# Kernel optimization log

Measured on AMD Instinct MI355X. Metric: run time of the kernel, lower is better.

Reference implementation:

```python
import jax, jax.numpy as jnp
import numpy as np

N = 16384; E = 262144; B = 8
IN = 768; HID = 256; H1 = 4; OUT = 128; H2 = 2

def setup_inputs() -> dict:
    key = jax.random.key(0)
    ks = jax.random.split(key, 16)
    s = 0.02
    def p(k, shape):
        return jax.random.normal(k, shape, jnp.float32) * s
    return {
        "x": jax.random.normal(ks[0], (N, IN), jnp.float32),
        "edge_index": jax.random.randint(ks[1], (2, E), 0, N),
        "batch": jnp.sort(jax.random.randint(ks[2], (N,), 0, B)),
        "W1": p(ks[3], (H1 * HID, IN)),
        "a_src1": p(ks[4], (H1, HID)),
        "a_dst1": p(ks[5], (H1, HID)),
        "b1": jnp.zeros((H1 * HID,), jnp.float32),
        "W2": p(ks[6], (H2 * OUT, H1 * HID)),
        "a_src2": p(ks[7], (H2, OUT)),
        "a_dst2": p(ks[8], (H2, OUT)),
        "b2": jnp.zeros((OUT,), jnp.float32),
        "proj_W": p(ks[9], (768, OUT)),
        "proj_b": jnp.zeros((768,), jnp.float32),
        "ln_g": jnp.ones((768,), jnp.float32),
        "ln_b": jnp.zeros((768,), jnp.float32),
        "rh_W1": p(ks[10], (32, OUT + 2)),
        "rh_b1": jnp.zeros((32,), jnp.float32),
        "rh_W2": p(ks[11], (1, 32)),
        "rh_b2": jnp.zeros((1,), jnp.float32),
        "num_graphs": B,
    }

def _gat(x, src, dst, W, a_s, a_d, bias, heads, ch, concat, n):
    # PyG GATConv (shared src/dst lin): h = x W^T -> [n, heads, ch]
    h = (x @ W.T).reshape(n, heads, ch)
    al_s = (h * a_s).sum(-1)  # [n, heads]
    al_d = (h * a_d).sum(-1)
    e = jax.nn.leaky_relu(al_s[src] + al_d[dst], 0.2)  # [E', heads]
    # segment softmax over incoming edges of each destination node
    m = jax.lax.stop_gradient(jax.ops.segment_max(e, dst, num_segments=n))
    ex = jnp.exp(e - m[dst])
    den = jax.ops.segment_sum(ex, dst, num_segments=n)
    w = ex / (den[dst] + 1e-16)
    out = jax.ops.segment_sum(w[:, :, None] * h[src], dst, num_segments=n)
    if concat:
        return out.reshape(n, heads * ch) + bias
    return out.mean(1) + bias

def reference(x, edge_index, batch, W1, a_src1, a_dst1, b1, W2, a_src2, a_dst2, b2,
              proj_W, proj_b, ln_g, ln_b, rh_W1, rh_b1, rh_W2, rh_b2, num_graphs):
    n = x.shape[0]
    src0, dst0 = edge_index[0], edge_index[1]
    loop = jnp.arange(n)  # GATConv adds self-loops by default
    src = jnp.concatenate([src0, loop])
    dst = jnp.concatenate([dst0, loop])
    h1 = jax.nn.elu(_gat(x, src, dst, W1, a_src1, a_dst1, b1, H1, HID, True, n))
    h2 = jax.nn.elu(_gat(h1, src, dst, W2, a_src2, a_dst2, b2, H2, OUT, False, n))
    # global mean pool per graph
    n_g = jax.ops.segment_sum(jnp.ones((n,), x.dtype), batch, num_segments=num_graphs)
    pooled = jax.ops.segment_sum(h2, batch, num_segments=num_graphs) / jnp.maximum(n_g, 1.0)[:, None]
    pe = pooled @ proj_W.T + proj_b
    mu = pe.mean(-1, keepdims=True)
    var = pe.var(-1, keepdims=True)
    struct_embed = (pe - mu) / jnp.sqrt(var + 1e-5) * ln_g + ln_b
    # topology stats from ORIGINAL edges (no self-loops), per original code
    e_g = jax.ops.segment_sum(jnp.ones((src0.shape[0],), x.dtype), batch[src0], num_segments=num_graphs)
    stats = jnp.stack([e_g / (n_g + 1e-6), jnp.log(n_g + 1.0)], axis=-1)  # [B, 2]
    ri = jnp.concatenate([pooled, stats], axis=-1)
    hid = jax.nn.relu(ri @ rh_W1.T + rh_b1)
    prop_risk = jax.nn.sigmoid(hid @ rh_W2.T + rh_b2)[:, 0]
    return struct_embed, h2, prop_risk
```

## Files before the change

kernel.cpp:

```cpp
#include <hip/hip_runtime.h>
#include <math.h>

#define NN    16384
#define EE    262144
#define ET    (EE + NN)
#define NB    8
#define IN_F  768
#define HID1  256
#define H1    4
#define D1    (H1*HID1)
#define OUT2  128
#define H2    2
#define D2    (H2*OUT2)

typedef __attribute__((ext_vector_type(8))) _Float16 f16x8;
typedef __attribute__((ext_vector_type(4))) float f32x4;

__device__ __forceinline__ float hf2f(unsigned short u) {
    union { unsigned short u; _Float16 h; } c; c.u = u; return (float)c.h;
}
__device__ __forceinline__ unsigned short f2hf(float f) {
    union { unsigned short u; _Float16 h; } c; c.h = (_Float16)f; return c.u;
}


__global__ void hist_kernel(const int* __restrict__ ei, const int* __restrict__ batch,
                            int* __restrict__ deg, int* __restrict__ n_g, int* __restrict__ e_cnt) {
    __shared__ int le[NB], ln[NB];
    int tid = threadIdx.x;
    if (tid < NB) { le[tid] = 0; ln[tid] = 0; }
    __syncthreads();
    int t = blockIdx.x * blockDim.x + tid;
    if (t < EE) {
        int s = ei[t];
        int d = ei[EE + t];
        atomicAdd(&deg[d], 1);
        atomicAdd(&le[batch[s]], 1);
    }
    if (t < NN) {
        atomicAdd(&ln[batch[t]], 1);
    }
    __syncthreads();
    if (tid < NB) {
        if (le[tid]) atomicAdd(&e_cnt[tid], le[tid]);
        if (ln[tid]) atomicAdd(&n_g[tid], ln[tid]);
    }
}

__global__ __launch_bounds__(1024) void scan_kernel(const int* __restrict__ deg, int* __restrict__ row_ptr) {
    __shared__ int sums[1024];
    int t = threadIdx.x;
    int base = t * 16;
    int local[16];
    int acc = 0;
#pragma unroll
    for (int i = 0; i < 16; i++) { local[i] = acc; acc += deg[base + i] + 1; }
    sums[t] = acc;
    __syncthreads();
    for (int off = 1; off < 1024; off <<= 1) {
        int v = (t >= off) ? sums[t - off] : 0;
        __syncthreads();
        sums[t] += v;
        __syncthreads();
    }
    int prev = (t == 0) ? 0 : sums[t - 1];
#pragma unroll
    for (int i = 0; i < 16; i++) row_ptr[base + i] = prev + local[i];
    if (t == 1023) row_ptr[NN] = sums[1023];
}

__global__ void scatter_kernel(const int* __restrict__ ei, const int* __restrict__ row_ptr,
                               int* __restrict__ cursor, int* __restrict__ colidx) {
    int t = blockIdx.x * blockDim.x + threadIdx.x;
    if (t >= ET) return;
    int s, d;
    if (t < EE) { s = ei[t]; d = ei[EE + t]; }
    else        { s = d = t - EE; }
    int pos = row_ptr[d] + atomicAdd(&cursor[d], 1);
    colidx[pos] = s;
}


__global__ void tohalf3_kernel(const float* __restrict__ x,  unsigned short* __restrict__ xo,
                               const float* __restrict__ w1, unsigned short* __restrict__ w1o,
                               const float* __restrict__ w2, unsigned short* __restrict__ w2o) {
    const int n1 = NN * IN_F / 4;
    const int n2 = D1 * IN_F / 4;
    const int n3 = D2 * D1 / 4;
    int i = blockIdx.x * blockDim.x + threadIdx.x;
    const float* src; unsigned short* dst; int j;
    if (i < n1)           { src = x;  dst = xo;  j = i; }
    else if (i < n1 + n2) { src = w1; dst = w1o; j = i - n1; }
    else if (i < n1 + n2 + n3) { src = w2; dst = w2o; j = i - n1 - n2; }
    else return;
    float4 v = ((const float4*)src)[j];
    ushort4 h;
    h.x = f2hf(v.x); h.y = f2hf(v.y); h.z = f2hf(v.z); h.w = f2hf(v.w);
    ((ushort4*)dst)[j] = h;
}


__device__ __forceinline__ void ld_lds16(const unsigned short* g, unsigned short* l) {
    __builtin_amdgcn_global_load_lds((__attribute__((address_space(1))) void*)g,
                                     (__attribute__((address_space(3))) void*)l, 16, 0, 0);
}

#define BM 128
#define BN 128
#define BK 32

__global__ __launch_bounds__(256) void gemm_mfma(const unsigned short* __restrict__ A,
                                                 const unsigned short* __restrict__ B,
                                                 unsigned short* __restrict__ C,
                                                 int M, int N, int K) {
    __shared__ __align__(16) unsigned short sA[BM * BK];
    __shared__ __align__(16) unsigned short sB[BN * BK];
    int t = threadIdx.x;
    int lane = t & 63, wave = t >> 6;

    int NC = N / BN;
    int b = blockIdx.x;
    int xcd = b & 7;
    int idx = b >> 3;
    int c = idx % NC;
    int rg = idx / NC;
    int bm = (rg * 8 + xcd) * BM;
    int bn = c * BN;

    int wm = (wave & 1) * 64, wn = (wave >> 1) * 64;

    const unsigned short* gbase;
    unsigned short* lbase;
    {
        int hrow = (wave & 1) * 64;
        if (wave < 2) { gbase = A + (size_t)(bm + hrow) * K; lbase = sA + hrow * BK; }
        else          { gbase = B + (size_t)(bn + hrow) * K; lbase = sB + hrow * BK; }
    }
    int schunk = (lane & 3) ^ ((lane >> 3) & 3);
    const unsigned short* gsrc = gbase + (size_t)(lane >> 2) * K + schunk * 8;

    f32x4 zero = {0.f, 0.f, 0.f, 0.f};
    f32x4 acc[4][4];
#pragma unroll
    for (int i = 0; i < 4; i++)
#pragma unroll
        for (int j = 0; j < 4; j++) acc[i][j] = zero;

    int row16 = lane & 15;
    int kq = ((lane >> 4) ^ ((row16 >> 1) & 3)) * 8;

    for (int k0 = 0; k0 < K; k0 += BK) {
#pragma unroll
        for (int i = 0; i < 4; i++)
            ld_lds16(gsrc + k0 + (size_t)(i * 16) * K, lbase + i * 16 * BK);
        __syncthreads();

        f16x8 ah[4], bh[4];
#pragma unroll
        for (int mt = 0; mt < 4; mt++)
            ah[mt] = *(const f16x8*)&sA[(wm + mt * 16 + row16) * BK + kq];
#pragma unroll
        for (int nt = 0; nt < 4; nt++)
            bh[nt] = *(const f16x8*)&sB[(wn + nt * 16 + row16) * BK + kq];
#pragma unroll
        for (int mt = 0; mt < 4; mt++)
#pragma unroll
            for (int nt = 0; nt < 4; nt++)
                acc[mt][nt] = __builtin_amdgcn_mfma_f32_16x16x32_f16(ah[mt], bh[nt], acc[mt][nt], 0, 0, 0);
        __syncthreads();
    }

    int crow0 = bm + wm + (lane >> 4) * 4;
    int ccol0 = bn + wn + row16;
#pragma unroll
    for (int mt = 0; mt < 4; mt++)
#pragma unroll
        for (int nt = 0; nt < 4; nt++)
#pragma unroll
            for (int reg = 0; reg < 4; reg++)
                C[(size_t)(crow0 + mt * 16 + reg) * N + ccol0 + nt * 16] = f2hf(acc[mt][nt][reg]);
}


__global__ __launch_bounds__(256) void al1_kernel(const unsigned short* __restrict__ h,
                                                  const float* __restrict__ a_s,
                                                  const float* __restrict__ a_d,
                                                  float* __restrict__ als,
                                                  float* __restrict__ ald) {
    int node = blockIdx.x;
    int head = threadIdx.x >> 6;
    int lane = threadIdx.x & 63;
    int co = head * HID1 + lane * 4;
    ushort4 hv = *(const ushort4*)(h + (size_t)node * D1 + co);
    float4 as = *(const float4*)(a_s + co);
    float4 ad = *(const float4*)(a_d + co);
    float h0 = hf2f(hv.x), h1 = hf2f(hv.y), h2 = hf2f(hv.z), h3 = hf2f(hv.w);
    float ss = h0 * as.x + h1 * as.y + h2 * as.z + h3 * as.w;
    float sd = h0 * ad.x + h1 * ad.y + h2 * ad.z + h3 * ad.w;
#pragma unroll
    for (int off = 32; off; off >>= 1) {
        ss += __shfl_down(ss, off);
        sd += __shfl_down(sd, off);
    }
    if (lane == 0) {
        als[node * H1 + head] = ss;
        ald[node * H1 + head] = sd;
    }
}

__global__ __launch_bounds__(256) void al2_kernel(const unsigned short* __restrict__ h,
                                                  const float* __restrict__ a_s,
                                                  const float* __restrict__ a_d,
                                                  float* __restrict__ als,
                                                  float* __restrict__ ald) {
    int unit = threadIdx.x >> 6;
    int node = blockIdx.x * 2 + (unit >> 1);
    int head = unit & 1;
    int lane = threadIdx.x & 63;
    int co = head * OUT2 + lane * 2;
    ushort2 hv = *(const ushort2*)(h + (size_t)node * D2 + co);
    float2 as = *(const float2*)(a_s + co);
    float2 ad = *(const float2*)(a_d + co);
    float h0 = hf2f(hv.x), h1 = hf2f(hv.y);
    float ss = h0 * as.x + h1 * as.y;
    float sd = h0 * ad.x + h1 * ad.y;
#pragma unroll
    for (int off = 32; off; off >>= 1) {
        ss += __shfl_down(ss, off);
        sd += __shfl_down(sd, off);
    }
    if (lane == 0) {
        als[node * H2 + head] = ss;
        ald[node * H2 + head] = sd;
    }
}

__device__ __forceinline__ float leaky(float v) { return v > 0.f ? v : 0.2f * v; }
__device__ __forceinline__ float elu1(float v) { return v > 0.f ? v : (__expf(v) - 1.f); }


__global__ __launch_bounds__(256) void agg1_kernel(const unsigned short* __restrict__ h,
                                                   const float* __restrict__ als,
                                                   const float* __restrict__ ald,
                                                   const int* __restrict__ row_ptr,
                                                   const int* __restrict__ colidx,
                                                   const float* __restrict__ bias,
                                                   unsigned short* __restrict__ outp) {
    int b = blockIdx.x;
    int s = b & 7;
    int g = b >> 3;
    int wave = threadIdx.x >> 6;
    int lane = threadIdx.x & 63;
    int lanesel = lane & 32;
    int l5 = lane & 31;
    int d = g * 8 + wave * 2 + (lanesel >> 5);
    int head = s >> 1;
    int start = row_ptr[d], end = row_ptr[d + 1];
    int deg = end - start;
    int degO = __shfl_xor(deg, 32);
    int degmax = max(deg, degO);
    float ald_h = ald[d * H1 + head];
    unsigned choff = (unsigned)(s * 128 + l5 * 4);

    float a0 = 0.f, a1 = 0.f, a2 = 0.f, a3 = 0.f;
    float wsum = 0.f;

    for (int c0 = 0; c0 < degmax; c0 += 32) {
        int ee = start + c0 + l5;
        int idx = ee < end ? ee : end - 1;
        int sL = colidx[idx];
        float ev = leaky(als[(sL << 2) + head] + ald_h);
        float wL = (ee < end) ? __expf(ev) : 0.f;
        float ws = wL;
        ws += __shfl_xor(ws, 16); ws += __shfl_xor(ws, 8);
        ws += __shfl_xor(ws, 4);  ws += __shfl_xor(ws, 2);  ws += __shfl_xor(ws, 1);
        wsum += ws;

        int n = degmax - c0; if (n > 32) n = 32;
        int n8 = (n + 7) & ~7;
        for (int k = 0; k < n8; k += 8) {
            ushort4 hv[8]; float wv[8];
#pragma unroll
            for (int j = 0; j < 8; j++) {
                int src = k + j + lanesel;
                int ssj = __shfl(sL, src);
                wv[j]   = __shfl(wL, src);
                hv[j] = *(const ushort4*)(h + (((unsigned)ssj << 10) + choff));
            }
#pragma unroll
            for (int j = 0; j < 8; j++) {
                float w = wv[j];
                a0 += w * hf2f(hv[j].x); a1 += w * hf2f(hv[j].y);
                a2 += w * hf2f(hv[j].z); a3 += w * hf2f(hv[j].w);
            }
        }
    }

    float sinv = 1.f / (wsum + 1e-16f);
    float4 bv = *(const float4*)(bias + s * 128 + l5 * 4);
    float o0 = elu1(a0 * sinv + bv.x);
    float o1 = elu1(a1 * sinv + bv.y);
    float o2 = elu1(a2 * sinv + bv.z);
    float o3 = elu1(a3 * sinv + bv.w);
    unsigned long long pk = (unsigned long long)f2hf(o0)
                          | ((unsigned long long)f2hf(o1) << 16)
                          | ((unsigned long long)f2hf(o2) << 32)
                          | ((unsigned long long)f2hf(o3) << 48);
    size_t o = (size_t)d * D1 + choff;
    __builtin_nontemporal_store(pk, (unsigned long long*)(outp + o));
}


__global__ __launch_bounds__(256) void agg2_kernel(const unsigned short* __restrict__ h,
                                                   const float* __restrict__ als,
                                                   const float* __restrict__ ald,
                                                   const int* __restrict__ row_ptr,
                                                   const int* __restrict__ colidx,
                                                   const float* __restrict__ bias,
                                                   float* __restrict__ out) {
    int wave = threadIdx.x >> 6;
    int lane = threadIdx.x & 63;
    int lanesel = lane & 32;
    int l5 = lane & 31;
    int head = lanesel >> 5;
    int d = blockIdx.x * 4 + wave;
    int start = row_ptr[d], end = row_ptr[d + 1];
    int deg = end - start;
    float ald_h = ald[d * H2 + head];
    unsigned ch4 = (unsigned)(lane << 2);

    float a0 = 0.f, a1 = 0.f, a2 = 0.f, a3 = 0.f;
    float wsum = 0.f;

    for (int c0 = 0; c0 < deg; c0 += 32) {
        int ee = start + c0 + l5;
        int idx = ee < end ? ee : end - 1;
        int sL = colidx[idx];
        float ev = leaky(als[(sL << 1) + head] + ald_h);
        float wL = (ee < end) ? __expf(ev) : 0.f;
        float ws = wL;
        ws += __shfl_xor(ws, 16); ws += __shfl_xor(ws, 8);
        ws += __shfl_xor(ws, 4);  ws += __shfl_xor(ws, 2);  ws += __shfl_xor(ws, 1);
        wsum += ws;

        int n = deg - c0; if (n > 32) n = 32;
        int n8 = (n + 7) & ~7;
        for (int k = 0; k < n8; k += 8) {
            ushort4 hv[8]; float wv[8];
#pragma unroll
            for (int j = 0; j < 8; j++) {
                int ssj = __builtin_amdgcn_readlane(sL, k + j);
                wv[j] = __shfl(wL, k + j + lanesel);
                hv[j] = *(const ushort4*)(h + (((unsigned)ssj << 8) + ch4));
            }
#pragma unroll
            for (int j = 0; j < 8; j++) {
                float w = wv[j];
                a0 += w * hf2f(hv[j].x); a1 += w * hf2f(hv[j].y);
                a2 += w * hf2f(hv[j].z); a3 += w * hf2f(hv[j].w);
            }
        }
    }

    float sinv = 1.f / (wsum + 1e-16f);
    float r0 = a0 * sinv, r1 = a1 * sinv, r2 = a2 * sinv, r3 = a3 * sinv;
    r0 += __shfl_xor(r0, 32);
    r1 += __shfl_xor(r1, 32);
    r2 += __shfl_xor(r2, 32);
    r3 += __shfl_xor(r3, 32);
    if (lane < 32) {
        float4 bv = *(const float4*)(bias + (l5 << 2));
        float4 o;
        o.x = elu1(r0 * 0.5f + bv.x);
        o.y = elu1(r1 * 0.5f + bv.y);
        o.z = elu1(r2 * 0.5f + bv.z);
        o.w = elu1(r3 * 0.5f + bv.w);
        *(float4*)(out + (size_t)d * OUT2 + (l5 << 2)) = o;
    }
}


__global__ __launch_bounds__(256) void pool_kernel(const float* __restrict__ h2,
                                                   const int* __restrict__ batch,
                                                   float* __restrict__ pooled) {
    int c = threadIdx.x & 127;
    int half = threadIdx.x >> 7;
    int n0 = blockIdx.x * 256 + half;
    int nend = blockIdx.x * 256 + 256;
    float acc = 0.f;
    int curg = batch[n0];
    for (int n = n0; n < nend; n += 2) {
        int g = batch[n];
        if (g != curg) {
            atomicAdd(&pooled[curg * OUT2 + c], acc);
            acc = 0.f; curg = g;
        }
        acc += h2[(size_t)n * OUT2 + c];
    }
    atomicAdd(&pooled[curg * OUT2 + c], acc);
}


__global__ __launch_bounds__(256) void final_kernel(const float* __restrict__ pooled_sum,
                                                    const int* __restrict__ n_g_i,
                                                    const int* __restrict__ e_cnt,
                                                    const float* __restrict__ projW,
                                                    const float* __restrict__ projb,
                                                    const float* __restrict__ lng,
                                                    const float* __restrict__ lnb,
                                                    const float* __restrict__ rhW1,
                                                    const float* __restrict__ rhb1,
                                                    const float* __restrict__ rhW2,
                                                    const float* __restrict__ rhb2,
                                                    float* __restrict__ out_se,
                                                    float* __restrict__ out_risk) {
    int b = blockIdx.x;
    int t = threadIdx.x;
    __shared__ float pooled[OUT2];
    __shared__ float pe[768];
    __shared__ float red[256];
    __shared__ float hid[32];
    __shared__ float stat_mu, stat_inv;

    float ng = (float)n_g_i[b];
    if (t < OUT2) pooled[t] = pooled_sum[b * OUT2 + t] / fmaxf(ng, 1.0f);
    __syncthreads();

    for (int j = t; j < 768; j += 256) {
        const float* wr = projW + (size_t)j * OUT2;
        float s = projb[j];
        for (int c = 0; c < OUT2; c++) s += pooled[c] * wr[c];
        pe[j] = s;
    }
    __syncthreads();

    float ls = 0.f, lq = 0.f;
    for (int j = t; j < 768; j += 256) { float v = pe[j]; ls += v; lq += v * v; }
    red[t] = ls;
    __syncthreads();
    for (int off = 128; off; off >>= 1) { if (t < off) red[t] += red[t + off]; __syncthreads(); }
    float tot = red[0];
    __syncthreads();
    red[t] = lq;
    __syncthreads();
    for (int off = 128; off; off >>= 1) { if (t < off) red[t] += red[t + off]; __syncthreads(); }
    float totq = red[0];
    if (t == 0) {
        float mu = tot / 768.f;
        float var = totq / 768.f - mu * mu;
        stat_mu = mu;
        stat_inv = 1.f / sqrtf(var + 1e-5f);
    }
    __syncthreads();
    float mu = stat_mu, inv = stat_inv;
    for (int j = t; j < 768; j += 256)
        out_se[(size_t)b * 768 + j] = (pe[j] - mu) * inv * lng[j] + lnb[j];

    float s0 = (float)e_cnt[b] / (ng + 1e-6f);
    float s1 = logf(ng + 1.0f);
    if (t < 32) {
        const float* wr = rhW1 + t * (OUT2 + 2);
        float s = rhb1[t];
        for (int c = 0; c < OUT2; c++) s += pooled[c] * wr[c];
        s += s0 * wr[OUT2] + s1 * wr[OUT2 + 1];
        hid[t] = fmaxf(s, 0.f);
    }
    __syncthreads();
    if (t == 0) {
        float s = rhb2[0];
        for (int k = 0; k < 32; k++) s += hid[k] * rhW2[k];
        out_risk[b] = 1.f / (1.f + __expf(-s));
    }
}


extern "C" void kernel_launch(void* const* d_in, const int* in_sizes, int n_in,
                              void* d_out, int out_size, void* d_ws, size_t ws_size,
                              hipStream_t stream) {
    const float* x     = (const float*)d_in[0];
    const int*   ei    = (const int*)  d_in[1];
    const int*   batch = (const int*)  d_in[2];
    const float* W1    = (const float*)d_in[3];
    const float* a_s1  = (const float*)d_in[4];
    const float* a_d1  = (const float*)d_in[5];
    const float* b1    = (const float*)d_in[6];
    const float* W2    = (const float*)d_in[7];
    const float* a_s2  = (const float*)d_in[8];
    const float* a_d2  = (const float*)d_in[9];
    const float* b2    = (const float*)d_in[10];
    const float* projW = (const float*)d_in[11];
    const float* projb = (const float*)d_in[12];
    const float* lng   = (const float*)d_in[13];
    const float* lnb   = (const float*)d_in[14];
    const float* rhW1  = (const float*)d_in[15];
    const float* rhb1  = (const float*)d_in[16];
    const float* rhW2  = (const float*)d_in[17];
    const float* rhb2  = (const float*)d_in[18];

    char* ws = (char*)d_ws;
    size_t off = 0;
    auto alloc = [&](size_t bytes) -> void* {
        void* p = ws + off;
        off += (bytes + 255) & ~(size_t)255;
        return p;
    };

    unsigned short* regionA = (unsigned short*)alloc((size_t)NN * D1 * 2);
    unsigned short* x_f  = regionA;
    unsigned short* h1a  = regionA;

    unsigned short* h1f  = (unsigned short*)alloc((size_t)NN * D1 * 2);
    unsigned short* h2ft = (unsigned short*)alloc((size_t)NN * D2 * 2);
    unsigned short* W1f  = (unsigned short*)alloc((size_t)D1 * IN_F * 2);
    unsigned short* W2f  = (unsigned short*)alloc((size_t)D2 * D1 * 2);
    float* als1   = (float*)alloc((size_t)NN * H1 * 4);
    float* ald1   = (float*)alloc((size_t)NN * H1 * 4);
    float* als2   = (float*)alloc((size_t)NN * H2 * 4);
    float* ald2   = (float*)alloc((size_t)NN * H2 * 4);
    int*   row_ptr= (int*)  alloc((size_t)(NN + 1) * 4);
    int*   colidx = (int*)  alloc((size_t)ET * 4);
    size_t zoff = off;
    int*   deg    = (int*)  alloc((size_t)NN * 4);
    int*   cursor = (int*)  alloc((size_t)NN * 4);
    int*   n_g    = (int*)  alloc((size_t)NB * 4);
    int*   e_cnt  = (int*)  alloc((size_t)NB * 4);
    float* pooled = (float*)alloc((size_t)NB * OUT2 * 4);
    size_t zbytes = off - zoff;

    float* out_se   = (float*)d_out;
    float* h2out    = out_se + NB * 768;
    float* out_risk = h2out + (size_t)NN * OUT2;

    hipMemsetAsync(ws + zoff, 0, zbytes, stream);

    hist_kernel<<<(EE + 255) / 256, 256, 0, stream>>>(ei, batch, deg, n_g, e_cnt);
    scan_kernel<<<1, 1024, 0, stream>>>(deg, row_ptr);
    scatter_kernel<<<(ET + 255) / 256, 256, 0, stream>>>(ei, row_ptr, cursor, colidx);

    {
        int ntot = NN * IN_F / 4 + D1 * IN_F / 4 + D2 * D1 / 4;
        tohalf3_kernel<<<(ntot + 255) / 256, 256, 0, stream>>>(x, x_f, W1, W1f, W2, W2f);
    }

    gemm_mfma<<<(NN / BM) * (D1 / BN), 256, 0, stream>>>(x_f, W1f, h1f, NN, D1, IN_F);
    al1_kernel<<<NN, 256, 0, stream>>>(h1f, a_s1, a_d1, als1, ald1);
    agg1_kernel<<<NN, 256, 0, stream>>>(h1f, als1, ald1, row_ptr, colidx, b1, h1a);

    gemm_mfma<<<(NN / BM) * (D2 / BN), 256, 0, stream>>>(h1a, W2f, h2ft, NN, D2, D1);
    al2_kernel<<<NN / 2, 256, 0, stream>>>(h2ft, a_s2, a_d2, als2, ald2);
    agg2_kernel<<<NN / 4, 256, 0, stream>>>(h2ft, als2, ald2, row_ptr, colidx, b2, h2out);

    pool_kernel<<<NN / 256, 256, 0, stream>>>(h2out, batch, pooled);

    final_kernel<<<NB, 256, 0, stream>>>(pooled, n_g, e_cnt, projW, projb, lng, lnb,
                                         rhW1, rhb1, rhW2, rhb2, out_se, out_risk);
}
```

Measured before the change: 397.5 us.

## Merge preprocessing and tail kernels with grid barriers to cut launches

Merges the memset into the fp16 conversion kernel and fuses histogram and scan into one persistent 256-block kernel using software grid barriers. The CSR scatter now runs as extra blocks of the first GEMM launch, and pooling and the final head share one kernel separated by a grid barrier. This removes several kernel launches and their serialization gaps. The cost is a reliance on all blocks being co-resident for the spin barriers, plus some serialized single-block work inside the fused kernels.

```diff
diff --git a/kernel.cpp b/kernel.cpp
--- a/kernel.cpp
+++ b/kernel.cpp
@@ -24,79 +24,109 @@
 }
 
 
-__global__ void hist_kernel(const int* __restrict__ ei, const int* __restrict__ batch,
-                            int* __restrict__ deg, int* __restrict__ n_g, int* __restrict__ e_cnt) {
+__device__ __forceinline__ void grid_barrier(int* cnt, int* gen, int nb) {
+    __syncthreads();
+    if (threadIdx.x == 0) {
+        int g = __hip_atomic_load(gen, __ATOMIC_RELAXED, __HIP_MEMORY_SCOPE_AGENT);
+        int v = __hip_atomic_fetch_add(cnt, 1, __ATOMIC_ACQ_REL, __HIP_MEMORY_SCOPE_AGENT);
+        if (v == nb - 1) {
+            __hip_atomic_store(cnt, 0, __ATOMIC_RELAXED, __HIP_MEMORY_SCOPE_AGENT);
+            __hip_atomic_fetch_add(gen, 1, __ATOMIC_RELEASE, __HIP_MEMORY_SCOPE_AGENT);
+        } else {
+            while (__hip_atomic_load(gen, __ATOMIC_ACQUIRE, __HIP_MEMORY_SCOPE_AGENT) == g)
+                __builtin_amdgcn_s_sleep(2);
+        }
+    }
+    __syncthreads();
+}
+
+
+__global__ void prep_kernel(const float* __restrict__ x,  unsigned short* __restrict__ xo,
+                            const float* __restrict__ w1, unsigned short* __restrict__ w1o,
+                            const float* __restrict__ w2, unsigned short* __restrict__ w2o,
+                            float4* __restrict__ zbase, int zunits) {
+    const int n1 = NN * IN_F / 4;
+    const int n2 = D1 * IN_F / 4;
+    const int n3 = D2 * D1 / 4;
+    int i = blockIdx.x * blockDim.x + threadIdx.x;
+    if (i < n1 + n2 + n3) {
+        const float* src; unsigned short* dst; int j;
+        if (i < n1)           { src = x;  dst = xo;  j = i; }
+        else if (i < n1 + n2) { src = w1; dst = w1o; j = i - n1; }
+        else                  { src = w2; dst = w2o; j = i - n1 - n2; }
+        float4 v = ((const float4*)src)[j];
+        ushort4 h;
+        h.x = f2hf(v.x); h.y = f2hf(v.y); h.z = f2hf(v.z); h.w = f2hf(v.w);
+        ((ushort4*)dst)[j] = h;
+    } else {
+        int j = i - (n1 + n2 + n3);
+        if (j < zunits) zbase[j] = make_float4(0.f, 0.f, 0.f, 0.f);
+    }
+}
+
+
+__global__ __launch_bounds__(256) void histscan_kernel(const int* __restrict__ ei,
+                                                       const int* __restrict__ batch,
+                                                       int* __restrict__ deg,
+                                                       int* __restrict__ n_g,
+                                                       int* __restrict__ e_cnt,
+                                                       int* __restrict__ row_ptr,
+                                                       int* __restrict__ bsum,
+                                                       int* bc, int* bg) {
     __shared__ int le[NB], ln[NB];
+    __shared__ int sc[256];
     int tid = threadIdx.x;
+    int b = blockIdx.x;
+
     if (tid < NB) { le[tid] = 0; ln[tid] = 0; }
     __syncthreads();
-    int t = blockIdx.x * blockDim.x + tid;
-    if (t < EE) {
+    for (int t = b * 256 + tid; t < EE; t += 256 * 256) {
         int s = ei[t];
         int d = ei[EE + t];
         atomicAdd(&deg[d], 1);
         atomicAdd(&le[batch[s]], 1);
-    }
-    if (t < NN) {
-        atomicAdd(&ln[batch[t]], 1);
+        if (t < NN) atomicAdd(&ln[batch[t]], 1);
     }
     __syncthreads();
     if (tid < NB) {
         if (le[tid]) atomicAdd(&e_cnt[tid], le[tid]);
         if (ln[tid]) atomicAdd(&n_g[tid], ln[tid]);
     }
-}
-
-__global__ __launch_bounds__(1024) void scan_kernel(const int* __restrict__ deg, int* __restrict__ row_ptr) {
-    __shared__ int sums[1024];
-    int t = threadIdx.x;
-    int base = t * 16;
-    int local[16];
-    int acc = 0;
-#pragma unroll
-    for (int i = 0; i < 16; i++) { local[i] = acc; acc += deg[base + i] + 1; }
-    sums[t] = acc;
-    __syncthreads();
-    for (int off = 1; off < 1024; off <<= 1) {
-        int v = (t >= off) ? sums[t - off] : 0;
+    grid_barrier(bc, bg, 256);
+
+    int node = b * 256 + tid;
+    if (b < 64) {
+        int v = __hip_atomic_load(&deg[node], __ATOMIC_RELAXED, __HIP_MEMORY_SCOPE_AGENT) + 1;
+        sc[tid] = v;
         __syncthreads();
-        sums[t] += v;
-        __syncthreads();
-    }
-    int prev = (t == 0) ? 0 : sums[t - 1];
-#pragma unroll
-    for (int i = 0; i < 16; i++) row_ptr[base + i] = prev + local[i];
-    if (t == 1023) row_ptr[NN] = sums[1023];
-}
-
-__global__ void scatter_kernel(const int* __restrict__ ei, const int* __restrict__ row_ptr,
-                               int* __restrict__ cursor, int* __restrict__ colidx) {
-    int t = blockIdx.x * blockDim.x + threadIdx.x;
-    if (t >= ET) return;
-    int s, d;
-    if (t < EE) { s = ei[t]; d = ei[EE + t]; }
-    else        { s = d = t - EE; }
-    int pos = row_ptr[d] + atomicAdd(&cursor[d], 1);
-    colidx[pos] = s;
-}
-
-
-__global__ void tohalf3_kernel(const float* __restrict__ x,  unsigned short* __restrict__ xo,
-                               const float* __restrict__ w1, unsigned short* __restrict__ w1o,
-                               const float* __restrict__ w2, unsigned short* __restrict__ w2o) {
-    const int n1 = NN * IN_F / 4;
-    const int n2 = D1 * IN_F / 4;
-    const int n3 = D2 * D1 / 4;
-    int i = blockIdx.x * blockDim.x + threadIdx.x;
-    const float* src; unsigned short* dst; int j;
-    if (i < n1)           { src = x;  dst = xo;  j = i; }
-    else if (i < n1 + n2) { src = w1; dst = w1o; j = i - n1; }
-    else if (i < n1 + n2 + n3) { src = w2; dst = w2o; j = i - n1 - n2; }
-    else return;
-    float4 v = ((const float4*)src)[j];
-    ushort4 h;
-    h.x = f2hf(v.x); h.y = f2hf(v.y); h.z = f2hf(v.z); h.w = f2hf(v.w);
-    ((ushort4*)dst)[j] = h;
+        for (int off = 1; off < 256; off <<= 1) {
+            int u = (tid >= off) ? sc[tid - off] : 0;
+            __syncthreads();
+            sc[tid] += u;
+            __syncthreads();
+        }
+        int incl = sc[tid];
+        row_ptr[node] = incl - v;
+        if (tid == 255)
+            __hip_atomic_store(&bsum[b], incl, __ATOMIC_RELAXED, __HIP_MEMORY_SCOPE_AGENT);
+    }
+    grid_barrier(bc, bg, 256);
+
+    if (b == 0 && tid < 64) {
+        int vv = __hip_atomic_load(&bsum[tid], __ATOMIC_RELAXED, __HIP_MEMORY_SCOPE_AGENT);
+        int e = vv;
+#pragma unroll
+        for (int off = 1; off < 64; off <<= 1) {
+            int u = __shfl_up(e, off);
+            if (tid >= off) e += u;
+        }
+        __hip_atomic_store(&bsum[tid], e - vv, __ATOMIC_RELAXED, __HIP_MEMORY_SCOPE_AGENT);
+        if (tid == 63) row_ptr[NN] = e;
+    }
+    grid_barrier(bc, bg, 256);
+
+    if (b < 64)
+        row_ptr[node] += __hip_atomic_load(&bsum[b], __ATOMIC_RELAXED, __HIP_MEMORY_SCOPE_AGENT);
 }
 
 
@@ -112,7 +142,24 @@
 __global__ __launch_bounds__(256) void gemm_mfma(const unsigned short* __restrict__ A,
                                                  const unsigned short* __restrict__ B,
                                                  unsigned short* __restrict__ C,
-                                                 int M, int N, int K) {
+                                                 int M, int N, int K,
+                                                 int gemmBlocks,
+                                                 const int* __restrict__ ei,
+                                                 const int* __restrict__ row_ptr,
+                                                 int* __restrict__ cursor,
+                                                 int* __restrict__ colidx) {
+    if ((int)blockIdx.x >= gemmBlocks) {
+        int t = (blockIdx.x - gemmBlocks) * 256 + threadIdx.x;
+        if (t < ET) {
+            int s, d;
+            if (t < EE) { s = ei[t]; d = ei[EE + t]; }
+            else        { s = d = t - EE; }
+            int pos = row_ptr[d] + atomicAdd(&cursor[d], 1);
+            colidx[pos] = s;
+        }
+        return;
+    }
+
     __shared__ __align__(16) unsigned short sA[BM * BK];
     __shared__ __align__(16) unsigned short sB[BN * BK];
     int t = threadIdx.x;
@@ -380,41 +427,22 @@
 }
 
 
-__global__ __launch_bounds__(256) void pool_kernel(const float* __restrict__ h2,
-                                                   const int* __restrict__ batch,
-                                                   float* __restrict__ pooled) {
-    int c = threadIdx.x & 127;
-    int half = threadIdx.x >> 7;
-    int n0 = blockIdx.x * 256 + half;
-    int nend = blockIdx.x * 256 + 256;
-    float acc = 0.f;
-    int curg = batch[n0];
-    for (int n = n0; n < nend; n += 2) {
-        int g = batch[n];
-        if (g != curg) {
-            atomicAdd(&pooled[curg * OUT2 + c], acc);
-            acc = 0.f; curg = g;
-        }
-        acc += h2[(size_t)n * OUT2 + c];
-    }
-    atomicAdd(&pooled[curg * OUT2 + c], acc);
-}
-
-
-__global__ __launch_bounds__(256) void final_kernel(const float* __restrict__ pooled_sum,
-                                                    const int* __restrict__ n_g_i,
-                                                    const int* __restrict__ e_cnt,
-                                                    const float* __restrict__ projW,
-                                                    const float* __restrict__ projb,
-                                                    const float* __restrict__ lng,
-                                                    const float* __restrict__ lnb,
-                                                    const float* __restrict__ rhW1,
-                                                    const float* __restrict__ rhb1,
-                                                    const float* __restrict__ rhW2,
-                                                    const float* __restrict__ rhb2,
-                                                    float* __restrict__ out_se,
-                                                    float* __restrict__ out_risk) {
-    int b = blockIdx.x;
+__global__ __launch_bounds__(256) void poolfinal_kernel(const float* __restrict__ h2,
+                                                        const int* __restrict__ batch,
+                                                        float* __restrict__ pooled_sum,
+                                                        const int* __restrict__ n_g_i,
+                                                        const int* __restrict__ e_cnt,
+                                                        const float* __restrict__ projW,
+                                                        const float* __restrict__ projb,
+                                                        const float* __restrict__ lng,
+                                                        const float* __restrict__ lnb,
+                                                        const float* __restrict__ rhW1,
+                                                        const float* __restrict__ rhb1,
+                                                        const float* __restrict__ rhW2,
+                                                        const float* __restrict__ rhb2,
+                                                        float* __restrict__ out_se,
+                                                        float* __restrict__ out_risk,
+                                                        int* bc, int* bg) {
     int t = threadIdx.x;
     __shared__ float pooled[OUT2];
     __shared__ float pe[768];
@@ -422,8 +450,33 @@
     __shared__ float hid[32];
     __shared__ float stat_mu, stat_inv;
 
-    float ng = (float)n_g_i[b];
-    if (t < OUT2) pooled[t] = pooled_sum[b * OUT2 + t] / fmaxf(ng, 1.0f);
+    {
+        int c = t & 127;
+        int half = t >> 7;
+        int n0 = blockIdx.x * 256 + half;
+        int nend = blockIdx.x * 256 + 256;
+        float acc = 0.f;
+        int curg = batch[n0];
+        for (int n = n0; n < nend; n += 2) {
+            int g = batch[n];
+            if (g != curg) {
+                atomicAdd(&pooled_sum[curg * OUT2 + c], acc);
+                acc = 0.f; curg = g;
+            }
+            acc += h2[(size_t)n * OUT2 + c];
+        }
+        atomicAdd(&pooled_sum[curg * OUT2 + c], acc);
+    }
+    grid_barrier(bc, bg, 64);
+    if (blockIdx.x >= NB) return;
+
+    int gb = blockIdx.x;
+    float ng = (float)n_g_i[gb];
+    if (t < OUT2) {
+        float ps = __hip_atomic_load(&pooled_sum[gb * OUT2 + t], __ATOMIC_RELAXED,
+                                     __HIP_MEMORY_SCOPE_AGENT);
+        pooled[t] = ps / fmaxf(ng, 1.0f);
+    }
     __syncthreads();
 
     for (int j = t; j < 768; j += 256) {
@@ -454,9 +507,9 @@
     __syncthreads();
     float mu = stat_mu, inv = stat_inv;
     for (int j = t; j < 768; j += 256)
-        out_se[(size_t)b * 768 + j] = (pe[j] - mu) * inv * lng[j] + lnb[j];
-
-    float s0 = (float)e_cnt[b] / (ng + 1e-6f);
+        out_se[(size_t)gb * 768 + j] = (pe[j] - mu) * inv * lng[j] + lnb[j];
+
+    float s0 = (float)e_cnt[gb] / (ng + 1e-6f);
     float s1 = logf(ng + 1.0f);
     if (t < 32) {
         const float* wr = rhW1 + t * (OUT2 + 2);
@@ -469,7 +522,7 @@
     if (t == 0) {
         float s = rhb2[0];
         for (int k = 0; k < 32; k++) s += hid[k] * rhW2[k];
-        out_risk[b] = 1.f / (1.f + __expf(-s));
+        out_risk[gb] = 1.f / (1.f + __expf(-s));
     }
 }
 
@@ -519,39 +572,51 @@
     float* ald2   = (float*)alloc((size_t)NN * H2 * 4);
     int*   row_ptr= (int*)  alloc((size_t)(NN + 1) * 4);
     int*   colidx = (int*)  alloc((size_t)ET * 4);
+    int*   bsum   = (int*)  alloc((size_t)64 * 4);
     size_t zoff = off;
     int*   deg    = (int*)  alloc((size_t)NN * 4);
     int*   cursor = (int*)  alloc((size_t)NN * 4);
     int*   n_g    = (int*)  alloc((size_t)NB * 4);
     int*   e_cnt  = (int*)  alloc((size_t)NB * 4);
     float* pooled = (float*)alloc((size_t)NB * OUT2 * 4);
+    int*   bars   = (int*)  alloc((size_t)8 * 4);
     size_t zbytes = off - zoff;
 
     float* out_se   = (float*)d_out;
     float* h2out    = out_se + NB * 768;
     float* out_risk = h2out + (size_t)NN * OUT2;
 
-    hipMemsetAsync(ws + zoff, 0, zbytes, stream);
-
-    hist_kernel<<<(EE + 255) / 256, 256, 0, stream>>>(ei, batch, deg, n_g, e_cnt);
-    scan_kernel<<<1, 1024, 0, stream>>>(deg, row_ptr);
-    scatter_kernel<<<(ET + 255) / 256, 256, 0, stream>>>(ei, row_ptr, cursor, colidx);
-
     {
         int ntot = NN * IN_F / 4 + D1 * IN_F / 4 + D2 * D1 / 4;
-        tohalf3_kernel<<<(ntot + 255) / 256, 256, 0, stream>>>(x, x_f, W1, W1f, W2, W2f);
-    }
-
-    gemm_mfma<<<(NN / BM) * (D1 / BN), 256, 0, stream>>>(x_f, W1f, h1f, NN, D1, IN_F);
+        int zunits = (int)(zbytes / 16);
+        int grid = (ntot + zunits + 255) / 256;
+        prep_kernel<<<grid, 256, 0, stream>>>(x, x_f, W1, W1f, W2, W2f,
+                                              (float4*)(ws + zoff), zunits);
+    }
+
+    histscan_kernel<<<256, 256, 0, stream>>>(ei, batch, deg, n_g, e_cnt, row_ptr, bsum,
+                                             &bars[0], &bars[1]);
+
+    {
+        int gb = (NN / BM) * (D1 / BN);
+        int sb = (ET + 255) / 256;
+        gemm_mfma<<<gb + sb, 256, 0, stream>>>(x_f, W1f, h1f, NN, D1, IN_F,
+                                               gb, ei, row_ptr, cursor, colidx);
+    }
+
     al1_kernel<<<NN, 256, 0, stream>>>(h1f, a_s1, a_d1, als1, ald1);
     agg1_kernel<<<NN, 256, 0, stream>>>(h1f, als1, ald1, row_ptr, colidx, b1, h1a);
 
-    gemm_mfma<<<(NN / BM) * (D2 / BN), 256, 0, stream>>>(h1a, W2f, h2ft, NN, D2, D1);
+    {
+        int gb = (NN / BM) * (D2 / BN);
+        gemm_mfma<<<gb, 256, 0, stream>>>(h1a, W2f, h2ft, NN, D2, D1,
+                                          gb, ei, row_ptr, cursor, colidx);
+    }
     al2_kernel<<<NN / 2, 256, 0, stream>>>(h2ft, a_s2, a_d2, als2, ald2);
     agg2_kernel<<<NN / 4, 256, 0, stream>>>(h2ft, als2, ald2, row_ptr, colidx, b2, h2out);
 
-    pool_kernel<<<NN / 256, 256, 0, stream>>>(h2out, batch, pooled);
-
-    final_kernel<<<NB, 256, 0, stream>>>(pooled, n_g, e_cnt, projW, projb, lng, lnb,
-                                         rhW1, rhb1, rhW2, rhb2, out_se, out_risk);
-}
+    poolfinal_kernel<<<NN / 256, 256, 0, stream>>>(h2out, batch, pooled, n_g, e_cnt,
+                                                   projW, projb, lng, lnb,
+                                                   rhW1, rhb1, rhW2, rhb2,
+                                                   out_se, out_risk, &bars[2], &bars[3]);
+}
```

After: 466.5 us. +17.4%, slower.
